# Optimization experiments

Measured on AMD Instinct MI355X. Metric: run time of the kernel, lower is better.

Reference implementation:

```python
import jax, jax.numpy as jnp
import numpy as np

RADIUS = 0.25
NUM_NEIGHBORS = 32
POS_DIM = 24
STEM_C = 64
PATCH_C = 256
LN_EPS = 1e-5


def query_ball_point(radius, nsample, xyz, new_xyz):
    # xyz: [B,N,3], new_xyz: [B,S,3] -> idx [B,S,nsample] (PointNet++ ball query)
    N = xyz.shape[1]
    sqr = (jnp.sum(new_xyz ** 2, -1)[:, :, None]
           + jnp.sum(xyz ** 2, -1)[:, None, :]
           - 2.0 * jnp.einsum('bsd,bnd->bsn', new_xyz, xyz))  # [B,S,N]
    idx = jnp.broadcast_to(jnp.arange(N, dtype=jnp.int32), sqr.shape)
    idx = jnp.where(sqr > radius * radius, N, idx)
    idx = jnp.sort(idx, axis=-1)[..., :nsample]  # first nsample in-ball (by index order)
    first = idx[..., :1]
    idx = jnp.where(idx == N, first, idx)  # pad empty slots with first neighbor
    return idx


def index_points(points, idx):
    # points [B,N,C], idx [B,S,K] -> [B,S,K,C]
    return jax.vmap(lambda p, i: p[i])(points, idx)


def rel_pos_encoding(rel_xyz, dim=POS_DIM):
    # sinusoidal Fourier encoding of 3D offsets: 3 coords * 2 (sin,cos) * dim//6 freqs
    nf = dim // 6
    freqs = 2.0 ** jnp.arange(nf, dtype=rel_xyz.dtype)
    ang = rel_xyz[..., None] * freqs  # [...,3,nf]
    enc = jnp.concatenate([jnp.sin(ang), jnp.cos(ang)], axis=-1)  # [...,3,2nf]
    return enc.reshape(rel_xyz.shape[:-1] + (dim,))


def point_mlp(x, W, b, gamma, beta, activate):
    h = jnp.einsum('...i,io->...o', x, W) + b
    mu = jnp.mean(h, -1, keepdims=True)
    var = jnp.mean((h - mu) ** 2, -1, keepdims=True)
    h = (h - mu) * jax.lax.rsqrt(var + LN_EPS) * gamma + beta
    return jax.nn.gelu(h, approximate=False) if activate else h


def setup_inputs() -> dict:
    key = jax.random.key(0)
    ks = jax.random.split(key, 8)
    B, N, S = 8, 16384, 1024
    in_c = STEM_C + 3 + POS_DIM  # 91
    return {
        'xyz': jax.random.uniform(ks[0], (B, N, 3), dtype=jnp.float32),
        'point_feature': jax.random.normal(ks[1], (B, N, STEM_C), dtype=jnp.float32),
        'patch_center': jax.random.uniform(ks[2], (B, S, 3), dtype=jnp.float32),
        'W1': jax.random.normal(ks[3], (in_c, PATCH_C), dtype=jnp.float32) * 0.02,
        'b1': jnp.zeros((PATCH_C,), jnp.float32),
        'g1': jnp.ones((PATCH_C,), jnp.float32),
        'be1': jnp.zeros((PATCH_C,), jnp.float32),
        'W2': jax.random.normal(ks[4], (PATCH_C, PATCH_C), dtype=jnp.float32) * 0.02,
        'b2': jnp.zeros((PATCH_C,), jnp.float32),
        'g2': jnp.ones((PATCH_C,), jnp.float32),
        'be2': jnp.zeros((PATCH_C,), jnp.float32),
    }


def reference(xyz, point_feature, patch_center, W1, b1, g1, be1, W2, b2, g2, be2):
    neighbor_idx = query_ball_point(RADIUS, NUM_NEIGHBORS, xyz, patch_center)  # [B,S,K]
    grouped_xyz = index_points(xyz, neighbor_idx)              # [B,S,K,3]
    grouped_feature = index_points(point_feature, neighbor_idx)  # [B,S,K,C]
    relative_xyz = grouped_xyz - patch_center[:, :, None, :]
    relative_position = rel_pos_encoding(relative_xyz)         # [B,S,K,24]
    grouped_input = jnp.concatenate((grouped_feature, relative_xyz, relative_position), axis=-1)
    h = point_mlp(grouped_input, W1, b1, g1, be1, True)
    h = point_mlp(h, W2, b2, g2, be2, False)
    patch_feature = jnp.max(h, axis=2)                         # max over neighbors -> [B,S,PATCH_C]
    return patch_feature, neighbor_idx
```

## Files before the change

### kernel.cpp

```cpp
#include <hip/hip_runtime.h>
#include <math.h>

#define NPTS 16384
#define KN 32
#define C 256
#define NQ 8192
#define PF_ELEMS (NQ * C)

#define W1P_ELEMS (3 * 16 * 64 * 8)
#define W2P_ELEMS (8 * 16 * 64 * 8)

typedef _Float16 half8 __attribute__((ext_vector_type(8)));
typedef _Float16 half4v __attribute__((ext_vector_type(4)));
typedef float f32x4 __attribute__((ext_vector_type(4)));

__global__ void prep_w_kernel(const float* __restrict__ W1,
                              const float* __restrict__ W2,
                              _Float16* __restrict__ wp) {
    const int e = blockIdx.x * 256 + threadIdx.x;
    if (e < W1P_ELEMS) {
        const int j = e & 7, lane = (e >> 3) & 63, nt = (e >> 9) & 15, kt = e >> 13;
        const int k = kt * 32 + (lane >> 4) * 8 + j;
        const int n = nt * 16 + (lane & 15);
        wp[e] = (_Float16)((k < 91) ? W1[k * C + n] : 0.0f);
    } else {
        const int e2 = e - W1P_ELEMS;
        const int j = e2 & 7, lane = (e2 >> 3) & 63, nt = (e2 >> 9) & 15, kt = e2 >> 13;
        const int k = kt * 32 + (lane >> 4) * 8 + j;
        const int n = nt * 16 + (lane & 15);
        wp[e] = (_Float16)W2[k * C + n];
    }
}

__device__ __forceinline__ float gelu_tanh(float x) {
    const float t  = x * x;
    const float p2 = fmaf(t, 0.0713548162726f, 1.59576912161f);
    const float e  = __expf(x * p2);
    return x - x * __builtin_amdgcn_rcpf(e + 1.0f);
}

__global__ void __launch_bounds__(256, 5)
encoder_fused(const float* __restrict__ xyz,
              const float* __restrict__ pf,
              const float* __restrict__ ctr,
              const float* __restrict__ b1, const float* __restrict__ g1,
              const float* __restrict__ be1,
              const float* __restrict__ b2, const float* __restrict__ g2,
              const float* __restrict__ be2,
              const _Float16* __restrict__ w1p,
              const _Float16* __restrict__ w2p,
              float* __restrict__ out0,
              float* __restrict__ out1) {
    const int q = blockIdx.x;
    const int b = q >> 10;
    const int t = threadIdx.x;
    const int w = t >> 6;
    const int lane = t & 63;
    const int quad = lane >> 4;
    const int l15  = lane & 15;

    __shared__ __align__(16) unsigned char H16raw[KN * 264 * 2];
    __shared__ __align__(16) unsigned char Xsraw[KN * 104 * 2];
    __shared__ float lnp[4 * 256];
    __shared__ int nbr[KN];
    __shared__ int wcnt[4];

    _Float16 (*H16)[264] = (_Float16(*)[264])H16raw;
    _Float16 (*Xs)[104]  = (_Float16(*)[104])Xsraw;
    float* lng1  = lnp;        float* lnbe1 = lnp + 256;
    float* lng2  = lnp + 512;  float* lnbe2 = lnp + 768;

    lnp[t]       = g1[t];  lnp[256 + t] = be1[t];
    lnp[512 + t] = g2[t];  lnp[768 + t] = be2[t];

    const float* xb = xyz + (size_t)b * NPTS * 3;
    const float cx = ctr[q * 3 + 0];
    const float cy = ctr[q * 3 + 1];
    const float cz = ctr[q * 3 + 2];
    const float sc = __fadd_rn(__fadd_rn(__fmul_rn(cx, cx), __fmul_rn(cy, cy)),
                               __fmul_rn(cz, cz));

    int found = 0;
    for (int base = 0; base < NPTS; base += 256) {
        const int n = base + t;
        const float px = xb[n * 3 + 0];
        const float py = xb[n * 3 + 1];
        const float pz = xb[n * 3 + 2];
        const float sp = __fadd_rn(__fadd_rn(__fmul_rn(px, px), __fmul_rn(py, py)),
                                   __fmul_rn(pz, pz));
        const float dt = __fadd_rn(__fadd_rn(__fmul_rn(cx, px), __fmul_rn(cy, py)),
                                   __fmul_rn(cz, pz));
        const float sqr = __fsub_rn(__fadd_rn(sc, sp), __fmul_rn(2.0f, dt));
        const bool inball = (sqr <= 0.0625f);

        const unsigned long long m = __ballot(inball);
        if (lane == 0) wcnt[w] = (int)__popcll(m);
        __syncthreads();
        int pre = found;
        if (w > 0) pre += wcnt[0];
        if (w > 1) pre += wcnt[1];
        if (w > 2) pre += wcnt[2];
        const int tot = found + wcnt[0] + wcnt[1] + wcnt[2] + wcnt[3];
        const int pos = pre + (int)__popcll(m & ((1ull << lane) - 1ull));
        if (inball && pos < KN) nbr[pos] = n;
        found = tot;
        __syncthreads();
        if (found >= KN) break;
    }
    const int count = (found < KN) ? found : KN;
    const int first = (count > 0) ? nbr[0] : NPTS;

    if (t < KN)
        out1[(size_t)q * KN + t] = (float)((t < count) ? nbr[t] : first);

    {
        const int k  = t >> 3;
        const int tc = t & 7;
        const int nidx = (k < count) ? nbr[k] : first;
        const int n = (nidx < NPTS) ? nidx : NPTS - 1;
        const float rx = xb[n * 3 + 0] - cx;
        const float ry = xb[n * 3 + 1] - cy;
        const float rz = xb[n * 3 + 2] - cz;
        const float* pfr = pf + ((size_t)b * NPTS + n) * 64;

        const float4 f0 = *(const float4*)(pfr + tc * 8);
        const float4 f1 = *(const float4*)(pfr + tc * 8 + 4);
        half8 hv;
        hv[0] = (_Float16)f0.x; hv[1] = (_Float16)f0.y;
        hv[2] = (_Float16)f0.z; hv[3] = (_Float16)f0.w;
        hv[4] = (_Float16)f1.x; hv[5] = (_Float16)f1.y;
        hv[6] = (_Float16)f1.z; hv[7] = (_Float16)f1.w;
        *(half8*)&Xs[k][tc * 8] = hv;

        half4v ov;
        #pragma unroll
        for (int j = 0; j < 4; ++j) {
            const int c = 64 + tc * 4 + j;
            float v;
            if (c < 67) {
                v = (c == 64) ? rx : ((c == 65) ? ry : rz);
            } else if (c < 91) {
                const int jj = c - 67;
                const int d = jj >> 3;
                const int mm = jj & 7;
                const float f = (float)(1 << (mm & 3));
                const float r = (d == 0) ? rx : ((d == 1) ? ry : rz);
                v = (mm < 4) ? __sinf(r * f) : __cosf(r * f);
            } else {
                v = 0.0f;
            }
            ov[j] = (_Float16)v;
        }
        *(half4v*)&Xs[k][64 + tc * 4] = ov;
    }
    __syncthreads();

    {
        f32x4 acc[2][4];
        #pragma unroll
        for (int mt = 0; mt < 2; ++mt)
            #pragma unroll
            for (int nt = 0; nt < 4; ++nt)
                acc[mt][nt] = (f32x4){0.f, 0.f, 0.f, 0.f};

        #pragma unroll
        for (int kt = 0; kt < 3; ++kt) {
            const half8 a0 = *(const half8*)&Xs[l15][kt * 32 + quad * 8];
            const half8 a1 = *(const half8*)&Xs[16 + l15][kt * 32 + quad * 8];
            #pragma unroll
            for (int nt = 0; nt < 4; ++nt) {
                const int ntg = w * 4 + nt;
                const half8 bf = *(const half8*)&w1p[((kt * 16 + ntg) * 64 + lane) * 8];
                acc[0][nt] = __builtin_amdgcn_mfma_f32_16x16x32_f16(a0, bf, acc[0][nt], 0, 0, 0);
                acc[1][nt] = __builtin_amdgcn_mfma_f32_16x16x32_f16(a1, bf, acc[1][nt], 0, 0, 0);
            }
        }
        #pragma unroll
        for (int nt = 0; nt < 4; ++nt) {
            const int col = w * 64 + nt * 16 + l15;
            const float bb = b1[col];
            #pragma unroll
            for (int mt = 0; mt < 2; ++mt)
                #pragma unroll
                for (int r = 0; r < 4; ++r)
                    H16[mt * 16 + quad * 4 + r][col] = (_Float16)(acc[mt][nt][r] + bb);
        }
    }
    __syncthreads();

    const int row = t >> 3;
    const int p   = t & 7;

    {
        _Float16* r0 = &H16[row][16 * p];
        _Float16* r1 = &H16[row][128 + 16 * p];
        const half8 h0 = *(const half8*)r0;
        const half8 h1 = *(const half8*)(r0 + 8);
        const half8 h2 = *(const half8*)r1;
        const half8 h3 = *(const half8*)(r1 + 8);

        float s = 0.0f, s2 = 0.0f;
        #pragma unroll
        for (int e = 0; e < 8; ++e) {
            const float x0 = (float)h0[e], x1 = (float)h1[e];
            const float x2 = (float)h2[e], x3 = (float)h3[e];
            s += (x0 + x1) + (x2 + x3);
            s2 = fmaf(x0, x0, fmaf(x1, x1, fmaf(x2, x2, fmaf(x3, x3, s2))));
        }
        #pragma unroll
        for (int off = 1; off < 8; off <<= 1) {
            s  += __shfl_xor(s, off, 64);
            s2 += __shfl_xor(s2, off, 64);
        }
        const float mu  = s * (1.0f / 256.0f);
        const float var = fmaf(s2, 1.0f / 256.0f, -mu * mu);
        const float rs  = __builtin_amdgcn_rsqf(var + 1e-5f);

        const int c0 = 16 * p, c1 = 128 + 16 * p;
        half8 o0, o1, o2, o3;
        #pragma unroll
        for (int e = 0; e < 8; ++e) {
            o0[e] = (_Float16)gelu_tanh(fmaf(((float)h0[e] - mu) * rs, lng1[c0 + e],     lnbe1[c0 + e]));
            o1[e] = (_Float16)gelu_tanh(fmaf(((float)h1[e] - mu) * rs, lng1[c0 + 8 + e], lnbe1[c0 + 8 + e]));
            o2[e] = (_Float16)gelu_tanh(fmaf(((float)h2[e] - mu) * rs, lng1[c1 + e],     lnbe1[c1 + e]));
            o3[e] = (_Float16)gelu_tanh(fmaf(((float)h3[e] - mu) * rs, lng1[c1 + 8 + e], lnbe1[c1 + 8 + e]));
        }
        *(half8*)r0       = o0;
        *(half8*)(r0 + 8) = o1;
        *(half8*)r1       = o2;
        *(half8*)(r1 + 8) = o3;
    }
    __syncthreads();

    {
        f32x4 acc[2][4];
        #pragma unroll
        for (int mt = 0; mt < 2; ++mt)
            #pragma unroll
            for (int nt = 0; nt < 4; ++nt)
                acc[mt][nt] = (f32x4){0.f, 0.f, 0.f, 0.f};

        #pragma unroll
        for (int kt = 0; kt < 8; ++kt) {
            const half8 a0 = *(const half8*)&H16[l15][kt * 32 + quad * 8];
            const half8 a1 = *(const half8*)&H16[16 + l15][kt * 32 + quad * 8];
            #pragma unroll
            for (int nt = 0; nt < 4; ++nt) {
                const int ntg = w * 4 + nt;
                const half8 bf = *(const half8*)&w2p[((kt * 16 + ntg) * 64 + lane) * 8];
                acc[0][nt] = __builtin_amdgcn_mfma_f32_16x16x32_f16(a0, bf, acc[0][nt], 0, 0, 0);
                acc[1][nt] = __builtin_amdgcn_mfma_f32_16x16x32_f16(a1, bf, acc[1][nt], 0, 0, 0);
            }
        }
        __syncthreads();
        #pragma unroll
        for (int nt = 0; nt < 4; ++nt) {
            const int col = w * 64 + nt * 16 + l15;
            const float bb = b2[col];
            #pragma unroll
            for (int mt = 0; mt < 2; ++mt)
                #pragma unroll
                for (int r = 0; r < 4; ++r)
                    H16[mt * 16 + quad * 4 + r][col] = (_Float16)(acc[mt][nt][r] + bb);
        }
    }
    __syncthreads();

    {
        _Float16* r0 = &H16[row][16 * p];
        _Float16* r1 = &H16[row][128 + 16 * p];
        const half8 h0 = *(const half8*)r0;
        const half8 h1 = *(const half8*)(r0 + 8);
        const half8 h2 = *(const half8*)r1;
        const half8 h3 = *(const half8*)(r1 + 8);

        float s = 0.0f, s2 = 0.0f;
        #pragma unroll
        for (int e = 0; e < 8; ++e) {
            const float x0 = (float)h0[e], x1 = (float)h1[e];
            const float x2 = (float)h2[e], x3 = (float)h3[e];
            s += (x0 + x1) + (x2 + x3);
            s2 = fmaf(x0, x0, fmaf(x1, x1, fmaf(x2, x2, fmaf(x3, x3, s2))));
        }
        #pragma unroll
        for (int off = 1; off < 8; off <<= 1) {
            s  += __shfl_xor(s, off, 64);
            s2 += __shfl_xor(s2, off, 64);
        }
        const float mu  = s * (1.0f / 256.0f);
        const float var = fmaf(s2, 1.0f / 256.0f, -mu * mu);
        const float rs  = __builtin_amdgcn_rsqf(var + 1e-5f);

        const int c0 = 16 * p, c1 = 128 + 16 * p;
        half8 o0, o1, o2, o3;
        #pragma unroll
        for (int e = 0; e < 8; ++e) {
            o0[e] = (_Float16)fmaf(((float)h0[e] - mu) * rs, lng2[c0 + e],     lnbe2[c0 + e]);
            o1[e] = (_Float16)fmaf(((float)h1[e] - mu) * rs, lng2[c0 + 8 + e], lnbe2[c0 + 8 + e]);
            o2[e] = (_Float16)fmaf(((float)h2[e] - mu) * rs, lng2[c1 + e],     lnbe2[c1 + e]);
            o3[e] = (_Float16)fmaf(((float)h3[e] - mu) * rs, lng2[c1 + 8 + e], lnbe2[c1 + 8 + e]);
        }
        *(half8*)r0       = o0;
        *(half8*)(r0 + 8) = o1;
        *(half8*)r1       = o2;
        *(half8*)(r1 + 8) = o3;
    }
    __syncthreads();

    {
        float m = -INFINITY;
        #pragma unroll
        for (int k = 0; k < KN; ++k)
            m = fmaxf(m, (float)H16[k][t]);
        out0[(size_t)q * C + t] = m;
    }
}

extern "C" void kernel_launch(void* const* d_in, const int* in_sizes, int n_in,
                              void* d_out, int out_size, void* d_ws, size_t ws_size,
                              hipStream_t stream) {
    const float* xyz = (const float*)d_in[0];
    const float* pf  = (const float*)d_in[1];
    const float* ctr = (const float*)d_in[2];
    const float* W1  = (const float*)d_in[3];
    const float* b1  = (const float*)d_in[4];
    const float* g1  = (const float*)d_in[5];
    const float* be1 = (const float*)d_in[6];
    const float* W2  = (const float*)d_in[7];
    const float* b2  = (const float*)d_in[8];
    const float* g2  = (const float*)d_in[9];
    const float* be2 = (const float*)d_in[10];

    float* out = (float*)d_out;
    _Float16* wp = (_Float16*)d_ws;

    prep_w_kernel<<<(W1P_ELEMS + W2P_ELEMS) / 256, 256, 0, stream>>>(W1, W2, wp);
    encoder_fused<<<NQ, 256, 0, stream>>>(xyz, pf, ctr,
                                          b1, g1, be1, b2, g2, be2,
                                          wp, wp + W1P_ELEMS,
                                          out, out + PF_ELEMS);
}
```

Before: 195.4 us.

## Fuse LayerNorm, GELU and max-pool into MFMA accumulator registers

```diff
diff --git a/kernel.cpp b/kernel.cpp
--- a/kernel.cpp
+++ b/kernel.cpp
@@ -9,6 +9,7 @@
 
 #define W1P_ELEMS (3 * 16 * 64 * 8)
 #define W2P_ELEMS (8 * 16 * 64 * 8)
+#define HSTR 264
 
 typedef _Float16 half8 __attribute__((ext_vector_type(8)));
 typedef _Float16 half4v __attribute__((ext_vector_type(4)));
@@ -59,14 +60,15 @@
     const int quad = lane >> 4;
     const int l15  = lane & 15;
 
-    __shared__ __align__(16) unsigned char H16raw[KN * 264 * 2];
+    __shared__ __align__(16) unsigned char H16raw[KN * HSTR * 2];
     __shared__ __align__(16) unsigned char Xsraw[KN * 104 * 2];
     __shared__ float lnp[4 * 256];
+    __shared__ __align__(16) float sums[KN][12];
     __shared__ int nbr[KN];
-    __shared__ int wcnt[4];
-
-    _Float16 (*H16)[264] = (_Float16(*)[264])H16raw;
-    _Float16 (*Xs)[104]  = (_Float16(*)[104])Xsraw;
+    __shared__ int wcnt[2][4];
+
+    _Float16 (*H16)[HSTR] = (_Float16(*)[HSTR])H16raw;
+    _Float16 (*Xs)[104]   = (_Float16(*)[104])Xsraw;
     float* lng1  = lnp;        float* lnbe1 = lnp + 256;
     float* lng2  = lnp + 512;  float* lnbe2 = lnp + 768;
 
@@ -81,6 +83,7 @@
                                __fmul_rn(cz, cz));
 
     int found = 0;
+    int par = 0;
     for (int base = 0; base < NPTS; base += 256) {
         const int n = base + t;
         const float px = xb[n * 3 + 0];
@@ -94,19 +97,20 @@
         const bool inball = (sqr <= 0.0625f);
 
         const unsigned long long m = __ballot(inball);
-        if (lane == 0) wcnt[w] = (int)__popcll(m);
+        if (lane == 0) wcnt[par][w] = (int)__popcll(m);
         __syncthreads();
         int pre = found;
-        if (w > 0) pre += wcnt[0];
-        if (w > 1) pre += wcnt[1];
-        if (w > 2) pre += wcnt[2];
-        const int tot = found + wcnt[0] + wcnt[1] + wcnt[2] + wcnt[3];
+        if (w > 0) pre += wcnt[par][0];
+        if (w > 1) pre += wcnt[par][1];
+        if (w > 2) pre += wcnt[par][2];
+        const int tot = found + wcnt[par][0] + wcnt[par][1] + wcnt[par][2] + wcnt[par][3];
         const int pos = pre + (int)__popcll(m & ((1ull << lane) - 1ull));
         if (inball && pos < KN) nbr[pos] = n;
         found = tot;
-        __syncthreads();
+        par ^= 1;
         if (found >= KN) break;
     }
+    __syncthreads();
     const int count = (found < KN) ? found : KN;
     const int first = (count > 0) ? nbr[0] : NPTS;
 
@@ -155,164 +159,195 @@
     }
     __syncthreads();
 
+    const int qx = (quad ^ (l15 >> 2)) * 8;
+
+    f32x4 acc[2][4];
+
+    #pragma unroll
+    for (int mt = 0; mt < 2; ++mt)
+        #pragma unroll
+        for (int nt = 0; nt < 4; ++nt)
+            acc[mt][nt] = (f32x4){0.f, 0.f, 0.f, 0.f};
+
+    #pragma unroll
+    for (int kt = 0; kt < 3; ++kt) {
+        const half8 a0 = *(const half8*)&Xs[l15][kt * 32 + quad * 8];
+        const half8 a1 = *(const half8*)&Xs[16 + l15][kt * 32 + quad * 8];
+        #pragma unroll
+        for (int nt = 0; nt < 4; ++nt) {
+            const int ntg = w * 4 + nt;
+            const half8 bf = *(const half8*)&w1p[((kt * 16 + ntg) * 64 + lane) * 8];
+            acc[0][nt] = __builtin_amdgcn_mfma_f32_16x16x32_f16(a0, bf, acc[0][nt], 0, 0, 0);
+            acc[1][nt] = __builtin_amdgcn_mfma_f32_16x16x32_f16(a1, bf, acc[1][nt], 0, 0, 0);
+        }
+    }
+
     {
-        f32x4 acc[2][4];
+        #pragma unroll
+        for (int nt = 0; nt < 4; ++nt) {
+            const float bb = b1[w * 64 + nt * 16 + l15];
+            #pragma unroll
+            for (int mt = 0; mt < 2; ++mt)
+                #pragma unroll
+                for (int r = 0; r < 4; ++r)
+                    acc[mt][nt][r] += bb;
+        }
+        float s[2][4], z[2][4];
         #pragma unroll
         for (int mt = 0; mt < 2; ++mt)
             #pragma unroll
-            for (int nt = 0; nt < 4; ++nt)
-                acc[mt][nt] = (f32x4){0.f, 0.f, 0.f, 0.f};
-
-        #pragma unroll
-        for (int kt = 0; kt < 3; ++kt) {
-            const half8 a0 = *(const half8*)&Xs[l15][kt * 32 + quad * 8];
-            const half8 a1 = *(const half8*)&Xs[16 + l15][kt * 32 + quad * 8];
-            #pragma unroll
-            for (int nt = 0; nt < 4; ++nt) {
-                const int ntg = w * 4 + nt;
-                const half8 bf = *(const half8*)&w1p[((kt * 16 + ntg) * 64 + lane) * 8];
-                acc[0][nt] = __builtin_amdgcn_mfma_f32_16x16x32_f16(a0, bf, acc[0][nt], 0, 0, 0);
-                acc[1][nt] = __builtin_amdgcn_mfma_f32_16x16x32_f16(a1, bf, acc[1][nt], 0, 0, 0);
-            }
-        }
-        #pragma unroll
-        for (int nt = 0; nt < 4; ++nt) {
-            const int col = w * 64 + nt * 16 + l15;
-            const float bb = b1[col];
+            for (int r = 0; r < 4; ++r) {
+                const float a = acc[mt][0][r], bb = acc[mt][1][r];
+                const float c = acc[mt][2][r], d = acc[mt][3][r];
+                s[mt][r] = (a + bb) + (c + d);
+                z[mt][r] = fmaf(a, a, fmaf(bb, bb, fmaf(c, c, d * d)));
+            }
+        #pragma unroll
+        for (int off = 1; off < 16; off <<= 1) {
+            #pragma unroll
+            for (int mt = 0; mt < 2; ++mt)
+                #pragma unroll
+                for (int r = 0; r < 4; ++r) {
+                    s[mt][r] += __shfl_xor(s[mt][r], off, 64);
+                    z[mt][r] += __shfl_xor(z[mt][r], off, 64);
+                }
+        }
+        if (l15 == 0) {
+            #pragma unroll
+            for (int mt = 0; mt < 2; ++mt)
+                #pragma unroll
+                for (int r = 0; r < 4; ++r) {
+                    const int row = 16 * mt + 4 * quad + r;
+                    float2 v; v.x = s[mt][r]; v.y = z[mt][r];
+                    *(float2*)&sums[row][2 * w] = v;
+                }
+        }
+        __syncthreads();
+        float mu[2][4], rs[2][4];
+        #pragma unroll
+        for (int mt = 0; mt < 2; ++mt)
+            #pragma unroll
+            for (int r = 0; r < 4; ++r) {
+                const int row = 16 * mt + 4 * quad + r;
+                const f32x4 v0 = *(const f32x4*)&sums[row][0];
+                const f32x4 v1 = *(const f32x4*)&sums[row][4];
+                const float ss = (v0.x + v0.z) + (v1.x + v1.z);
+                const float qq = (v0.y + v0.w) + (v1.y + v1.w);
+                const float m  = ss * (1.0f / 256.0f);
+                const float va = fmaf(qq, 1.0f / 256.0f, -m * m);
+                mu[mt][r] = m;
+                rs[mt][r] = __builtin_amdgcn_rsqf(va + 1e-5f);
+            }
+        #pragma unroll
+        for (int nt = 0; nt < 4; ++nt) {
+            const int col  = w * 64 + nt * 16 + l15;
+            const int colp = col ^ (quad << 3);
+            const float g  = lng1[col];
+            const float be = lnbe1[col];
+            #pragma unroll
+            for (int mt = 0; mt < 2; ++mt)
+                #pragma unroll
+                for (int r = 0; r < 4; ++r) {
+                    const float y = fmaf((acc[mt][nt][r] - mu[mt][r]) * rs[mt][r], g, be);
+                    H16[16 * mt + 4 * quad + r][colp] = (_Float16)gelu_tanh(y);
+                }
+        }
+    }
+    __syncthreads();
+
+    #pragma unroll
+    for (int mt = 0; mt < 2; ++mt)
+        #pragma unroll
+        for (int nt = 0; nt < 4; ++nt)
+            acc[mt][nt] = (f32x4){0.f, 0.f, 0.f, 0.f};
+
+    #pragma unroll
+    for (int kt = 0; kt < 8; ++kt) {
+        const half8 a0 = *(const half8*)&H16[l15][kt * 32 + qx];
+        const half8 a1 = *(const half8*)&H16[16 + l15][kt * 32 + qx];
+        #pragma unroll
+        for (int nt = 0; nt < 4; ++nt) {
+            const int ntg = w * 4 + nt;
+            const half8 bf = *(const half8*)&w2p[((kt * 16 + ntg) * 64 + lane) * 8];
+            acc[0][nt] = __builtin_amdgcn_mfma_f32_16x16x32_f16(a0, bf, acc[0][nt], 0, 0, 0);
+            acc[1][nt] = __builtin_amdgcn_mfma_f32_16x16x32_f16(a1, bf, acc[1][nt], 0, 0, 0);
+        }
+    }
+
+    {
+        #pragma unroll
+        for (int nt = 0; nt < 4; ++nt) {
+            const float bb = b2[w * 64 + nt * 16 + l15];
             #pragma unroll
             for (int mt = 0; mt < 2; ++mt)
                 #pragma unroll
                 for (int r = 0; r < 4; ++r)
-                    H16[mt * 16 + quad * 4 + r][col] = (_Float16)(acc[mt][nt][r] + bb);
-        }
-    }
-    __syncthreads();
-
-    const int row = t >> 3;
-    const int p   = t & 7;
-
-    {
-        _Float16* r0 = &H16[row][16 * p];
-        _Float16* r1 = &H16[row][128 + 16 * p];
-        const half8 h0 = *(const half8*)r0;
-        const half8 h1 = *(const half8*)(r0 + 8);
-        const half8 h2 = *(const half8*)r1;
-        const half8 h3 = *(const half8*)(r1 + 8);
-
-        float s = 0.0f, s2 = 0.0f;
-        #pragma unroll
-        for (int e = 0; e < 8; ++e) {
-            const float x0 = (float)h0[e], x1 = (float)h1[e];
-            const float x2 = (float)h2[e], x3 = (float)h3[e];
-            s += (x0 + x1) + (x2 + x3);
-            s2 = fmaf(x0, x0, fmaf(x1, x1, fmaf(x2, x2, fmaf(x3, x3, s2))));
-        }
-        #pragma unroll
-        for (int off = 1; off < 8; off <<= 1) {
-            s  += __shfl_xor(s, off, 64);
-            s2 += __shfl_xor(s2, off, 64);
-        }
-        const float mu  = s * (1.0f / 256.0f);
-        const float var = fmaf(s2, 1.0f / 256.0f, -mu * mu);
-        const float rs  = __builtin_amdgcn_rsqf(var + 1e-5f);
-
-        const int c0 = 16 * p, c1 = 128 + 16 * p;
-        half8 o0, o1, o2, o3;
-        #pragma unroll
-        for (int e = 0; e < 8; ++e) {
-            o0[e] = (_Float16)gelu_tanh(fmaf(((float)h0[e] - mu) * rs, lng1[c0 + e],     lnbe1[c0 + e]));
-            o1[e] = (_Float16)gelu_tanh(fmaf(((float)h1[e] - mu) * rs, lng1[c0 + 8 + e], lnbe1[c0 + 8 + e]));
-            o2[e] = (_Float16)gelu_tanh(fmaf(((float)h2[e] - mu) * rs, lng1[c1 + e],     lnbe1[c1 + e]));
-            o3[e] = (_Float16)gelu_tanh(fmaf(((float)h3[e] - mu) * rs, lng1[c1 + 8 + e], lnbe1[c1 + 8 + e]));
-        }
-        *(half8*)r0       = o0;
-        *(half8*)(r0 + 8) = o1;
-        *(half8*)r1       = o2;
-        *(half8*)(r1 + 8) = o3;
-    }
-    __syncthreads();
-
-    {
-        f32x4 acc[2][4];
+                    acc[mt][nt][r] += bb;
+        }
+        float s[2][4], z[2][4];
         #pragma unroll
         for (int mt = 0; mt < 2; ++mt)
             #pragma unroll
-            for (int nt = 0; nt < 4; ++nt)
-                acc[mt][nt] = (f32x4){0.f, 0.f, 0.f, 0.f};
-
-        #pragma unroll
-        for (int kt = 0; kt < 8; ++kt) {
-            const half8 a0 = *(const half8*)&H16[l15][kt * 32 + quad * 8];
-            const half8 a1 = *(const half8*)&H16[16 + l15][kt * 32 + quad * 8];
-            #pragma unroll
-            for (int nt = 0; nt < 4; ++nt) {
-                const int ntg = w * 4 + nt;
-                const half8 bf = *(const half8*)&w2p[((kt * 16 + ntg) * 64 + lane) * 8];
-                acc[0][nt] = __builtin_amdgcn_mfma_f32_16x16x32_f16(a0, bf, acc[0][nt], 0, 0, 0);
-                acc[1][nt] = __builtin_amdgcn_mfma_f32_16x16x32_f16(a1, bf, acc[1][nt], 0, 0, 0);
-            }
+            for (int r = 0; r < 4; ++r) {
+                const float a = acc[mt][0][r], bb = acc[mt][1][r];
+                const float c = acc[mt][2][r], d = acc[mt][3][r];
+                s[mt][r] = (a + bb) + (c + d);
+                z[mt][r] = fmaf(a, a, fmaf(bb, bb, fmaf(c, c, d * d)));
+            }
+        #pragma unroll
+        for (int off = 1; off < 16; off <<= 1) {
+            #pragma unroll
+            for (int mt = 0; mt < 2; ++mt)
+                #pragma unroll
+                for (int r = 0; r < 4; ++r) {
+                    s[mt][r] += __shfl_xor(s[mt][r], off, 64);
+                    z[mt][r] += __shfl_xor(z[mt][r], off, 64);
+                }
+        }
+        if (l15 == 0) {
+            #pragma unroll
+            for (int mt = 0; mt < 2; ++mt)
+                #pragma unroll
+                for (int r = 0; r < 4; ++r) {
+                    const int row = 16 * mt + 4 * quad + r;
+                    float2 v; v.x = s[mt][r]; v.y = z[mt][r];
+                    *(float2*)&sums[row][2 * w] = v;
+                }
         }
         __syncthreads();
-        #pragma unroll
-        for (int nt = 0; nt < 4; ++nt) {
-            const int col = w * 64 + nt * 16 + l15;
-            const float bb = b2[col];
-            #pragma unroll
-            for (int mt = 0; mt < 2; ++mt)
-                #pragma unroll
-                for (int r = 0; r < 4; ++r)
-                    H16[mt * 16 + quad * 4 + r][col] = (_Float16)(acc[mt][nt][r] + bb);
-        }
-    }
-    __syncthreads();
-
-    {
-        _Float16* r0 = &H16[row][16 * p];
-        _Float16* r1 = &H16[row][128 + 16 * p];
-        const half8 h0 = *(const half8*)r0;
-        const half8 h1 = *(const half8*)(r0 + 8);
-        const half8 h2 = *(const half8*)r1;
-        const half8 h3 = *(const half8*)(r1 + 8);
-
-        float s = 0.0f, s2 = 0.0f;
-        #pragma unroll
-        for (int e = 0; e < 8; ++e) {
-            const float x0 = (float)h0[e], x1 = (float)h1[e];
-            const float x2 = (float)h2[e], x3 = (float)h3[e];
-            s += (x0 + x1) + (x2 + x3);
-            s2 = fmaf(x0, x0, fmaf(x1, x1, fmaf(x2, x2, fmaf(x3, x3, s2))));
-        }
-        #pragma unroll
-        for (int off = 1; off < 8; off <<= 1) {
-            s  += __shfl_xor(s, off, 64);
-            s2 += __shfl_xor(s2, off, 64);
-        }
-        const float mu  = s * (1.0f / 256.0f);
-        const float var = fmaf(s2, 1.0f / 256.0f, -mu * mu);
-        const float rs  = __builtin_amdgcn_rsqf(var + 1e-5f);
-
-        const int c0 = 16 * p, c1 = 128 + 16 * p;
-        half8 o0, o1, o2, o3;
-        #pragma unroll
-        for (int e = 0; e < 8; ++e) {
-            o0[e] = (_Float16)fmaf(((float)h0[e] - mu) * rs, lng2[c0 + e],     lnbe2[c0 + e]);
-            o1[e] = (_Float16)fmaf(((float)h1[e] - mu) * rs, lng2[c0 + 8 + e], lnbe2[c0 + 8 + e]);
-            o2[e] = (_Float16)fmaf(((float)h2[e] - mu) * rs, lng2[c1 + e],     lnbe2[c1 + e]);
-            o3[e] = (_Float16)fmaf(((float)h3[e] - mu) * rs, lng2[c1 + 8 + e], lnbe2[c1 + 8 + e]);
-        }
-        *(half8*)r0       = o0;
-        *(half8*)(r0 + 8) = o1;
-        *(half8*)r1       = o2;
-        *(half8*)(r1 + 8) = o3;
-    }
-    __syncthreads();
-
-    {
-        float m = -INFINITY;
-        #pragma unroll
-        for (int k = 0; k < KN; ++k)
-            m = fmaxf(m, (float)H16[k][t]);
-        out0[(size_t)q * C + t] = m;
+        float mu[2][4], rs[2][4];
+        #pragma unroll
+        for (int mt = 0; mt < 2; ++mt)
+            #pragma unroll
+            for (int r = 0; r < 4; ++r) {
+                const int row = 16 * mt + 4 * quad + r;
+                const f32x4 v0 = *(const f32x4*)&sums[row][0];
+                const f32x4 v1 = *(const f32x4*)&sums[row][4];
+                const float ss = (v0.x + v0.z) + (v1.x + v1.z);
+                const float qq = (v0.y + v0.w) + (v1.y + v1.w);
+                const float m  = ss * (1.0f / 256.0f);
+                const float va = fmaf(qq, 1.0f / 256.0f, -m * m);
+                mu[mt][r] = m;
+                rs[mt][r] = __builtin_amdgcn_rsqf(va + 1e-5f);
+            }
+        #pragma unroll
+        for (int nt = 0; nt < 4; ++nt) {
+            const int col  = w * 64 + nt * 16 + l15;
+            const float g  = lng2[col];
+            const float be = lnbe2[col];
+            float mx = -INFINITY;
+            #pragma unroll
+            for (int mt = 0; mt < 2; ++mt)
+                #pragma unroll
+                for (int r = 0; r < 4; ++r) {
+                    const float y = fmaf((acc[mt][nt][r] - mu[mt][r]) * rs[mt][r], g, be);
+                    mx = fmaxf(mx, y);
+                }
+            mx = fmaxf(mx, __shfl_xor(mx, 16, 64));
+            mx = fmaxf(mx, __shfl_xor(mx, 32, 64));
+            if (quad == 0)
+                out0[(size_t)q * C + col] = mx;
+        }
     }
 }
 
```

Measured after the change: 212.8 us. +8.9%, slower.
